# Optimization experiments

Hardware: AMD Instinct MI355X
Metric: run time of the kernel (lower is better)

## Reference

```python
import jax, jax.numpy as jnp
import numpy as np
import math

N = 6000      # nodes
E = 96000     # edges
HID = 32      # hidden_dim
DEPTH = 3
RATIO = 0.2
BN_EPS = 1e-5


def _gcn(x, A, W, b):
    # GCNConv(improved=True): A_hat = A + 2I, out = D^-1/2 A_hat D^-1/2 (x W) + b
    # A[i, j] = weight of edge j -> i (message-passing orientation)
    n = A.shape[0]
    idx = jnp.arange(n)
    Ah = A.at[idx, idx].add(2.0)
    deg = Ah.sum(axis=1)
    dinv = jnp.where(deg > 0, jax.lax.rsqrt(deg), 0.0)
    An = dinv[:, None] * Ah * dinv[None, :]
    return An @ (x @ W) + b


def _two_hop(A):
    # GraphUNet.augment_adj: add self loops, sparse A@A, remove self loops
    n = A.shape[0]
    idx = jnp.arange(n)
    A1 = A.at[idx, idx].add(1.0)
    A2 = A1 @ A1
    return A2.at[idx, idx].set(0.0)


def _unpack(fl):
    x = fl[0]
    wd = list(fl[1:9:2]); bd = list(fl[2:9:2])
    pv = list(fl[9:12])
    wu = list(fl[12:18:2]); bu = list(fl[13:18:2])
    return x, (wd, bd, pv, wu, bu, fl[18], fl[19])


def _forward(x, edge_index, params):
    wd, bd, pv, wu, bu, bn_g, bn_b = params
    n = x.shape[0]
    # dense adjacency, transposed so A[dst, src] = edge weight
    A = jnp.zeros((n, n), x.dtype).at[edge_index[1], edge_index[0]].add(1.0)
    h = jax.nn.relu(_gcn(x, A, wd[0], bd[0]))
    xs, As, perms = [h], [A], []
    Acur = A
    for i in range(DEPTH):
        A2 = _two_hop(Acur)
        # TopKPooling: score = tanh(x.p / ||p||), keep top ceil(ratio*n)
        p = pv[i]
        score = jnp.tanh((h @ p) / jnp.linalg.norm(p))
        k = math.ceil(RATIO * h.shape[0])
        vals, perm = jax.lax.top_k(score, k)
        h = h[perm] * vals[:, None]
        Acur = A2[perm][:, perm]
        h = jax.nn.relu(_gcn(h, Acur, wd[i + 1], bd[i + 1]))
        if i < DEPTH - 1:
            xs.append(h)
            As.append(Acur)
        perms.append(perm)
    for i in range(DEPTH):
        j = DEPTH - 1 - i
        up = jnp.zeros_like(xs[j]).at[perms[j]].set(h)  # unpool
        h = _gcn(xs[j] + up, As[j], wu[i], bu[i])       # sum_res=True
        if i < DEPTH - 1:
            h = jax.nn.relu(h)
    # PFNet5 tail: BatchNorm1d(1) (batch stats) + sigmoid on channel 0
    v = h[:, 0]
    mean = v.mean()
    var = jnp.mean((v - mean) ** 2)
    r1 = jax.nn.sigmoid(bn_g[0] * (v - mean) * jax.lax.rsqrt(var + BN_EPS) + bn_b[0])
    return h.at[:, 0].set(r1)


def setup_inputs() -> dict:
    key = jax.random.key(0)
    ks = jax.random.split(key, 20)
    def nrm(k, shape, s=0.1):
        return jax.random.normal(k, shape, jnp.float32) * s
    inp = {
        "x": jax.random.normal(ks[0], (N, 3), jnp.float32),
        "edge_index": jax.random.randint(ks[1], (2, E), 0, N),
    }
    dims_down = [(3, HID), (HID, HID), (HID, HID), (HID, HID)]
    for i, (di, do) in enumerate(dims_down):
        inp[f"w_down{i}"] = nrm(ks[2 + i], (di, do))
        inp[f"b_down{i}"] = jnp.zeros((do,), jnp.float32)
    for i in range(3):
        inp[f"pool{i}"] = nrm(ks[6 + i], (HID,))
    dims_up = [(HID, HID), (HID, HID), (HID, 4)]
    for i, (di, do) in enumerate(dims_up):
        inp[f"w_up{i}"] = nrm(ks[9 + i], (di, do))
        inp[f"b_up{i}"] = jnp.zeros((do,), jnp.float32)
    inp["bn_gamma"] = jnp.ones((1,), jnp.float32)
    inp["bn_beta"] = jnp.zeros((1,), jnp.float32)
    return inp


def reference(x, edge_index, w_down0, b_down0, w_down1, b_down1, w_down2, b_down2,
              w_down3, b_down3, pool0, pool1, pool2, w_up0, b_up0, w_up1, b_up1,
              w_up2, b_up2, bn_gamma, bn_beta):
    fl = (x, w_down0, b_down0, w_down1, b_down1, w_down2, b_down2, w_down3, b_down3,
          pool0, pool1, pool2, w_up0, b_up0, w_up1, b_up1, w_up2, b_up2,
          bn_gamma, bn_beta)
    x_, params = _unpack(fl)
    return _forward(x_, edge_index, params)
```

## Files before the change

### kernel.cpp

```cpp
#include <hip/hip_runtime.h>
#include <hip/hip_bf16.h>

#define TPB 256

__global__ void k_count(const int* __restrict__ ei, int E, int* __restrict__ cnt){
  int e = blockIdx.x*blockDim.x + threadIdx.x;
  if(e < E) atomicAdd(&cnt[ei[E + e]], 1);
}

template<int IPT>
__global__ void k_scan(const int* __restrict__ cnt, int n, int* __restrict__ rowptr){
  int tid = threadIdx.x;
  int base = tid * IPT;
  int loc[IPT]; int s = 0;
  #pragma unroll
  for(int q = 0; q < IPT; ++q){ int i = base + q; int v = (i < n) ? cnt[i] : 0; s += v; loc[q] = s; }
  int lane = tid & 63, w = tid >> 6;
  int ss = s;
  #pragma unroll
  for(int o = 1; o < 64; o <<= 1){ int t = __shfl_up(ss, o, 64); if(lane >= o) ss += t; }
  __shared__ int wsum[16];
  if(lane == 63) wsum[w] = ss;
  __syncthreads();
  if(tid < 16){
    int t = wsum[tid];
    for(int o = 1; o < 16; o <<= 1){ int u = __shfl_up(t, o, 64); if(tid >= o) t += u; }
    wsum[tid] = t;
  }
  __syncthreads();
  int excl = ss - s + (w > 0 ? wsum[w-1] : 0);
  if(tid == 0) rowptr[0] = 0;
  #pragma unroll
  for(int q = 0; q < IPT; ++q){ int i = base + q; if(i < n) rowptr[i+1] = excl + loc[q]; }
}

__global__ void k_fill(const int* __restrict__ ei, int E, const int* __restrict__ rowptr,
                       int* __restrict__ fill, int* __restrict__ colidx){
  int e = blockIdx.x*blockDim.x + threadIdx.x;
  if(e >= E) return;
  int d = ei[E + e], s = ei[e];
  int p = rowptr[d] + atomicAdd(&fill[d], 1);
  colidx[p] = s;
}

__global__ void k_mm_dinv(const float* __restrict__ h, const float* __restrict__ W,
                          const float* __restrict__ dinv, const int* __restrict__ cnt,
                          float* __restrict__ dinv_out, float* __restrict__ out,
                          int n, int cin, int cout){
  int t = blockIdx.x*blockDim.x + threadIdx.x;
  if(t >= n*cout) return;
  int i = t / cout, c = t - i*cout;
  float dv;
  if(cnt){ dv = rsqrtf((float)cnt[i] + 2.0f); if(c == 0) dinv_out[i] = dv; }
  else dv = dinv[i];
  float s = 0.f;
  for(int d = 0; d < cin; ++d) s += h[i*cin + d] * W[d*cout + c];
  out[t] = dv * s;
}

template<int COUT>
__global__ void k_addup_mm(const float* __restrict__ base, const float* __restrict__ h,
                           const int* __restrict__ rank, const float* __restrict__ W,
                           const float* __restrict__ dinv, float* __restrict__ out, int n){
  int t = blockIdx.x*blockDim.x + threadIdx.x;
  if(t >= n*COUT) return;
  int i = t / COUT, c = t - i*COUT;
  int r = rank[i];
  const float* br = base + (size_t)i*32;
  const float* hr = h + (size_t)(r >= 0 ? r : 0)*32;
  float s = 0.f;
  #pragma unroll
  for(int d = 0; d < 32; ++d){
    float z = br[d] + ((r >= 0) ? hr[d] : 0.f);
    s += z * W[d*COUT + c];
  }
  out[t] = dinv[i] * s;
}

template<int C, bool RELU, bool SCORE>
__global__ void k_csr_gcn(const int* __restrict__ rowptr, const int* __restrict__ colidx,
                          const float* __restrict__ xwd, const float* __restrict__ dinv,
                          const float* __restrict__ bias, float* __restrict__ out, int n,
                          const float* __restrict__ pvec, float* __restrict__ score){
  int t = blockIdx.x*blockDim.x + threadIdx.x;
  if(t >= n*C) return;
  int i = t / C, c = t % C;
  float acc = 2.0f * xwd[i*C + c];
  int b = rowptr[i], e = rowptr[i+1];
  for(int p = b; p < e; ++p) acc += xwd[colidx[p]*C + c];
  float y = dinv[i]*acc + bias[c];
  y = RELU ? fmaxf(y, 0.f) : y;
  out[t] = y;
  if(SCORE){
    float pv = pvec[c];
    float sd = y*pv, nn = pv*pv;
    #pragma unroll
    for(int o = 16; o > 0; o >>= 1){ sd += __shfl_xor(sd, o, 32); nn += __shfl_xor(nn, o, 32); }
    if(c == 0) score[i] = tanhf(sd / sqrtf(nn));
  }
}

template<int NMAX>
__global__ __launch_bounds__(1024)
void k_pool_radix(const float* __restrict__ score, const float* __restrict__ h,
                  int n, int k, int* __restrict__ perm, int* __restrict__ rank,
                  float* __restrict__ hout){
  __shared__ unsigned keys[NMAX];
  __shared__ int bins[2048];
  __shared__ int wsum[16];
  __shared__ unsigned s_prefix;
  __shared__ int s_rk, s_found, s_cntgt;
  int tid = threadIdx.x, lane = tid & 63, w = tid >> 6;

  for(int i = tid; i < n; i += 1024){
    rank[i] = -1;
    unsigned u = __float_as_uint(score[i]);
    u ^= (u & 0x80000000u) ? 0xFFFFFFFFu : 0x80000000u;
    keys[i] = u;
  }
  if(tid == 0){ s_prefix = 0u; s_rk = k; }
  __syncthreads();

  for(int pass = 0; pass < 3; ++pass){
    const int width = (pass < 2) ? 11 : 10;
    const int shift = (pass == 0) ? 21 : ((pass == 1) ? 10 : 0);
    const int nb = 1 << width;
    for(int b2 = tid; b2 < nb; b2 += 1024) bins[b2] = 0;
    __syncthreads();
    unsigned prefix = s_prefix;
    int rk = s_rk;
    const int hs = shift + width;
    for(int i = tid; i < n; i += 1024){
      unsigned kk = keys[i];
      bool match = (pass == 0) || ((kk >> hs) == (prefix >> hs));
      if(match) atomicAdd(&bins[(kk >> shift) & (nb-1)], 1);
    }
    __syncthreads();
    int ipt = (nb + 1023) >> 10;
    int loc0 = 0, loc1 = 0, s = 0;
    { int r = tid*ipt; int v = (r < nb) ? bins[nb-1-r] : 0; s += v; loc0 = s;
      if(ipt == 2){ int r2 = r+1; int v2 = (r2 < nb) ? bins[nb-1-r2] : 0; s += v2; loc1 = s; } }
    int ss = s;
    #pragma unroll
    for(int o = 1; o < 64; o <<= 1){ int t2 = __shfl_up(ss, o, 64); if(lane >= o) ss += t2; }
    if(lane == 63) wsum[w] = ss;
    __syncthreads();
    if(tid < 16){
      int t2 = wsum[tid];
      #pragma unroll
      for(int o = 1; o < 16; o <<= 1){ int u2 = __shfl_up(t2, o, 64); if(tid >= o) t2 += u2; }
      wsum[tid] = t2;
    }
    __syncthreads();
    int excl = ss - s + (w ? wsum[w-1] : 0);
    { int r = tid*ipt; if(r < nb) bins[nb-1-r] = excl + loc0;
      if(ipt == 2){ int r2 = r+1; if(r2 < nb) bins[nb-1-r2] = excl + loc1; } }
    __syncthreads();
    for(int b2 = tid; b2 < nb; b2 += 1024){
      int cge = bins[b2];
      int cgt = (b2+1 < nb) ? bins[b2+1] : 0;
      if(cge >= rk && cgt < rk){ s_found = b2; s_cntgt = cgt; }
    }
    __syncthreads();
    if(tid == 0){ s_prefix |= ((unsigned)s_found) << shift; s_rk -= s_cntgt; }
    __syncthreads();
  }
  unsigned T = s_prefix;
  int r = s_rk;
  int cgt_total = k - r;

  int CH = (n + 1023) >> 10;
  int base = tid*CH, c_gt = 0, c_eq = 0;
  for(int q = 0; q < CH; ++q){
    int i = base+q;
    if(i < n){ unsigned u = keys[i]; c_gt += (u > T); c_eq += (u == T); }
  }
  int packed = c_gt*8192 + c_eq;
  int ss2 = packed;
  #pragma unroll
  for(int o = 1; o < 64; o <<= 1){ int t2 = __shfl_up(ss2, o, 64); if(lane >= o) ss2 += t2; }
  if(lane == 63) wsum[w] = ss2;
  __syncthreads();
  if(tid < 16){
    int t2 = wsum[tid];
    #pragma unroll
    for(int o = 1; o < 16; o <<= 1){ int u2 = __shfl_up(t2, o, 64); if(tid >= o) t2 += u2; }
    wsum[tid] = t2;
  }
  __syncthreads();
  int excl2 = ss2 - packed + (w ? wsum[w-1] : 0);
  int gt_before = excl2 / 8192, eq_before = excl2 % 8192;
  for(int q = 0; q < CH; ++q){
    int i = base+q;
    if(i >= n) continue;
    unsigned u = keys[i];
    if(u > T){ int pos = gt_before++; perm[pos] = i; rank[i] = pos; }
    else if(u == T){
      int tr = eq_before++;
      if(tr < r){ int pos = cgt_total + tr; perm[pos] = i; rank[i] = pos; }
    }
  }
  __syncthreads();
  for(int t = tid; t < k*32; t += 1024){
    int i = t >> 5, c = t & 31;
    int idx = perm[i];
    hout[t] = h[(size_t)idx*32 + c] * score[idx];
  }
}

__global__ __launch_bounds__(256)
void k_build_B1(const int* __restrict__ rowptr, const int* __restrict__ colidx,
                const int* __restrict__ perm1, const int* __restrict__ rank1, int K1,
                float* __restrict__ dinv1, int* __restrict__ rowbeg, int* __restrict__ rowend,
                int* __restrict__ col1, float* __restrict__ val1, int* __restrict__ cursor){
  __shared__ float row[1216];
  __shared__ int wsum[4];
  __shared__ float fs[4];
  __shared__ int s_base;
  int tid = threadIdx.x, lane = tid & 63, w = tid >> 6;
  int i = blockIdx.x;
  for(int j = tid; j < K1; j += 256) row[j] = 0.f;
  __syncthreads();
  int d = perm1[i];
  int b = rowptr[d], len = rowptr[d+1]-b;
  for(int p = tid; p < len; p += 256){
    int s = colidx[b+p]; int rs = rank1[s];
    if(rs >= 0) atomicAdd(&row[rs], 2.0f);
  }
  for(int ww = tid; ww < len*8; ww += 256){
    int p = ww >> 3, sub = ww & 7;
    int s = colidx[b+p];
    for(int q = rowptr[s]+sub, qe = rowptr[s+1]; q < qe; q += 8){
      int r2 = rank1[colidx[q]];
      if(r2 >= 0) atomicAdd(&row[r2], 1.0f);
    }
  }
  __syncthreads();
  if(tid == 0) row[i] = 0.f;
  __syncthreads();
  float s = 0.f;
  for(int j = tid; j < K1; j += 256) s += row[j];
  for(int o = 32; o > 0; o >>= 1) s += __shfl_down(s, o, 64);
  if(lane == 0) fs[w] = s;
  __syncthreads();
  if(tid == 0){
    dinv1[i] = rsqrtf(fs[0]+fs[1]+fs[2]+fs[3] + 2.0f);
    row[i] = 1.0f;
  }
  __syncthreads();
  int CH = (K1 + 255) >> 8;
  int base = tid*CH, cnt = 0;
  for(int q = 0; q < CH; ++q){ int j = base+q; if(j < K1 && row[j] != 0.f) ++cnt; }
  int ss = cnt;
  #pragma unroll
  for(int o = 1; o < 64; o <<= 1){ int t2 = __shfl_up(ss, o, 64); if(lane >= o) ss += t2; }
  if(lane == 63) wsum[w] = ss;
  __syncthreads();
  if(tid < 4){
    int t2 = wsum[tid];
    for(int o = 1; o < 4; o <<= 1){ int u2 = __shfl_up(t2, o, 64); if(tid >= o) t2 += u2; }
    wsum[tid] = t2;
  }
  __syncthreads();
  if(tid == 0) s_base = atomicAdd(cursor, wsum[3]);
  __syncthreads();
  int off = s_base + ss - cnt + (w ? wsum[w-1] : 0);
  for(int q = 0; q < CH; ++q){
    int j = base+q;
    if(j < K1 && row[j] != 0.f){ col1[off] = j; val1[off] = row[j]; ++off; }
  }
  if(tid == 0){ rowbeg[i] = s_base; rowend[i] = s_base + wsum[3]; }
}

template<bool RELU, bool SCORE>
__global__ void k_spmm_gcn(const int* __restrict__ rb, const int* __restrict__ re,
                           const int* __restrict__ ci, const float* __restrict__ cv,
                           const float* __restrict__ hwd, const float* __restrict__ dinv,
                           const float* __restrict__ bias, float* __restrict__ out, int n,
                           const float* __restrict__ pvec, float* __restrict__ score){
  int t = blockIdx.x*blockDim.x + threadIdx.x;
  if(t >= n*32) return;
  int i = t >> 5, c = t & 31;
  float acc = hwd[i*32 + c];
  for(int p = rb[i], e = re[i]; p < e; ++p) acc += cv[p]*hwd[ci[p]*32 + c];
  float y = dinv[i]*acc + bias[c];
  y = RELU ? fmaxf(y, 0.f) : y;
  out[t] = y;
  if(SCORE){
    float pv = pvec[c];
    float sd = y*pv, nn = pv*pv;
    #pragma unroll
    for(int o = 16; o > 0; o >>= 1){ sd += __shfl_xor(sd, o, 32); nn += __shfl_xor(nn, o, 32); }
    if(c == 0) score[i] = tanhf(sd / sqrtf(nn));
  }
}

__global__ __launch_bounds__(256)
void k_twohop_sp(const int* __restrict__ rb, const int* __restrict__ re,
                 const int* __restrict__ ci, const float* __restrict__ cv,
                 const int* __restrict__ perm2, const int* __restrict__ rank2,
                 float* __restrict__ C2, float* __restrict__ dinv2, int K2){
  __shared__ float acc[256];
  __shared__ float fs[4];
  int i = blockIdx.x, tid = threadIdx.x, lane = tid & 63, w = tid >> 6;
  for(int j = tid; j < K2; j += 256) acc[j] = 0.f;
  __syncthreads();
  int qi = perm2[i];
  int b = rb[qi], len = re[qi]-b;
  for(int ww = tid; ww < len*8; ww += 256){
    int p = b + (ww >> 3), sub = ww & 7;
    int t = ci[p]; float v = cv[p];
    for(int q = rb[t] + sub, qe = re[t]; q < qe; q += 8){
      int j = rank2[ci[q]];
      if(j >= 0) atomicAdd(&acc[j], v*cv[q]);
    }
  }
  __syncthreads();
  if(tid == 0) acc[i] = 0.f;
  __syncthreads();
  float s = 0.f;
  for(int j = tid; j < K2; j += 256) s += acc[j];
  for(int o = 32; o > 0; o >>= 1) s += __shfl_down(s, o, 64);
  if(lane == 0) fs[w] = s;
  __syncthreads();
  if(tid == 0) dinv2[i] = rsqrtf(fs[0]+fs[1]+fs[2]+fs[3] + 2.0f);
  for(int j = tid; j < K2; j += 256) C2[(size_t)i*K2 + j] = acc[j];
}

template<bool RELU, bool SCORE>
__global__ void k_dgcn_row(const float* __restrict__ C, const float* __restrict__ hwd,
                           const float* __restrict__ dinv, const float* __restrict__ bias,
                           float* __restrict__ out, int n,
                           const float* __restrict__ pvec, float* __restrict__ score){
  __shared__ float sh[8][32];
  int i = blockIdx.x;
  int c = threadIdx.x & 31, s = threadIdx.x >> 5;
  const float* row = C + (size_t)i*n;
  float acc = 0.f;
  for(int t = s; t < n; t += 8) acc += row[t]*hwd[t*32 + c];
  sh[s][c] = acc;
  __syncthreads();
  if(s == 0){
    float a = sh[0][c]+sh[1][c]+sh[2][c]+sh[3][c]+sh[4][c]+sh[5][c]+sh[6][c]+sh[7][c];
    a += 2.f*hwd[i*32 + c];
    float y = dinv[i]*a + bias[c];
    y = RELU ? fmaxf(y, 0.f) : y;
    out[i*32 + c] = y;
    if(SCORE){
      float pv = pvec[c];
      float sd = y*pv, nn = pv*pv;
      #pragma unroll
      for(int o = 16; o > 0; o >>= 1){ sd += __shfl_xor(sd, o, 32); nn += __shfl_xor(nn, o, 32); }
      if(c == 0) score[i] = tanhf(sd / sqrtf(nn));
    }
  }
}

__global__ __launch_bounds__(256)
void k_twohop_d3(const float* __restrict__ C2, int n, const int* __restrict__ perm3,
                 int k, float* __restrict__ C3, float* __restrict__ dinv3){
  __shared__ float acc[4][64];
  int i = blockIdx.x, tid = threadIdx.x;
  int col = tid & 63, st = tid >> 6;
  int qi = perm3[i];
  int qj = (col < k) ? perm3[col] : 0;
  float a = 0.f;
  if(col < k){
    for(int tt = st; tt < n; tt += 4){
      float av = C2[(size_t)qi*n + tt] + ((tt == qi) ? 1.f : 0.f);
      float bv = C2[(size_t)tt*n + qj] + ((tt == qj) ? 1.f : 0.f);
      a += av * bv;
    }
  }
  acc[st][col] = a;
  __syncthreads();
  if(st == 0){
    float v = acc[0][col]+acc[1][col]+acc[2][col]+acc[3][col];
    if(col == i) v = 0.f;
    if(col < k) C3[(size_t)i*k + col] = v;
    float sv = (col < k) ? v : 0.f;
    for(int o = 32; o > 0; o >>= 1) sv += __shfl_down(sv, o, 64);
    if(col == 0) dinv3[i] = rsqrtf(sv + 2.0f);
  }
}

__global__ void k_bn(float* __restrict__ out, int n, const float* __restrict__ g,
                     const float* __restrict__ b){
  __shared__ float sh[16];
  __shared__ float sval;
  int tid = threadIdx.x, lane = tid & 63, w = tid >> 6;
  int nw = blockDim.x >> 6;
  float s = 0.f;
  for(int i = tid; i < n; i += blockDim.x) s += out[i*4];
  for(int o = 32; o > 0; o >>= 1) s += __shfl_down(s, o, 64);
  if(lane == 0) sh[w] = s;
  __syncthreads();
  if(tid == 0){ float t = 0.f; for(int q = 0; q < nw; ++q) t += sh[q]; sval = t / n; }
  __syncthreads();
  float mean = sval;
  float v = 0.f;
  for(int i = tid; i < n; i += blockDim.x){ float d = out[i*4] - mean; v += d*d; }
  for(int o = 32; o > 0; o >>= 1) v += __shfl_down(v, o, 64);
  __syncthreads();
  if(lane == 0) sh[w] = v;
  __syncthreads();
  if(tid == 0){ float t = 0.f; for(int q = 0; q < nw; ++q) t += sh[q]; sval = t / n; }
  __syncthreads();
  float var = sval;
  float scale = g[0] * rsqrtf(var + 1e-5f);
  float beta = b[0];
  for(int i = tid; i < n; i += blockDim.x){
    float r = scale*(out[i*4] - mean) + beta;
    out[i*4] = 1.f / (1.f + expf(-r));
  }
}

extern "C" void kernel_launch(void* const* d_in, const int* in_sizes, int n_in,
                              void* d_out, int out_size, void* d_ws, size_t ws_size,
                              hipStream_t stream){
  const float* x  =(const float*)d_in[0];
  const int*   ei =(const int*)  d_in[1];
  const float* W0 =(const float*)d_in[2];  const float* b0 =(const float*)d_in[3];
  const float* W1 =(const float*)d_in[4];  const float* b1 =(const float*)d_in[5];
  const float* W2 =(const float*)d_in[6];  const float* b2 =(const float*)d_in[7];
  const float* W3 =(const float*)d_in[8];  const float* b3 =(const float*)d_in[9];
  const float* p0 =(const float*)d_in[10];
  const float* p1 =(const float*)d_in[11];
  const float* p2 =(const float*)d_in[12];
  const float* Wu0=(const float*)d_in[13]; const float* bu0=(const float*)d_in[14];
  const float* Wu1=(const float*)d_in[15]; const float* bu1=(const float*)d_in[16];
  const float* Wu2=(const float*)d_in[17]; const float* bu2=(const float*)d_in[18];
  const float* bng=(const float*)d_in[19]; const float* bnb=(const float*)d_in[20];
  float* out = (float*)d_out;

  const int n0 = in_sizes[0] / 3;
  const int E  = in_sizes[1] / 2;
  const int K1 = (n0 + 4) / 5;
  const int K2 = (K1 + 4) / 5;
  const int K3 = (K2 + 4) / 5;
  const int CAP1 = 512*1024;

  char* wsp = (char*)d_ws; size_t off = 0;
  auto alloc = [&](size_t bytes)->char*{
    char* p = wsp + off; off = (off + bytes + 255) & ~((size_t)255); return p;
  };

  int*   zreg   = (int*)  alloc((size_t)(2*n0+64)*4);
  int*   cnt    = zreg;
  int*   fill   = zreg + n0;
  int*   cursor = zreg + 2*n0;
  int*   rowptr = (int*)  alloc((size_t)(n0+1)*4);
  int*   colidx = (int*)  alloc((size_t)E*4);
  float* dinv0  = (float*)alloc((size_t)n0*4);
  float* hwd    = (float*)alloc((size_t)n0*32*4);
  float* h0     = (float*)alloc((size_t)n0*32*4);
  float* score  = (float*)alloc((size_t)n0*4);
  int*   perm1  = (int*)  alloc((size_t)K1*4);
  int*   rank1  = (int*)  alloc((size_t)n0*4);
  float* h1p    = (float*)alloc((size_t)K1*32*4);
  float* dinv1  = (float*)alloc((size_t)K1*4);
  int*   rowbeg1= (int*)  alloc((size_t)K1*4);
  int*   rowend1= (int*)  alloc((size_t)K1*4);
  int*   col1   = (int*)  alloc((size_t)CAP1*4);
  float* val1   = (float*)alloc((size_t)CAP1*4);
  float* h1     = (float*)alloc((size_t)K1*32*4);
  int*   perm2  = (int*)  alloc((size_t)K2*4);
  int*   rank2  = (int*)  alloc((size_t)K1*4);
  float* h2p    = (float*)alloc((size_t)K2*32*4);
  float* C2     = (float*)alloc((size_t)K2*K2*4);
  float* dinv2  = (float*)alloc((size_t)K2*4);
  float* h2     = (float*)alloc((size_t)K2*32*4);
  int*   perm3  = (int*)  alloc((size_t)K3*4);
  int*   rank3  = (int*)  alloc((size_t)K2*4);
  float* h3p    = (float*)alloc((size_t)K3*32*4);
  float* C3     = (float*)alloc((size_t)K3*K3*4);
  float* dinv3  = (float*)alloc((size_t)K3*4);
  float* h3     = (float*)alloc((size_t)K3*32*4);
  float* hu2    = (float*)alloc((size_t)K2*32*4);
  float* hu1    = (float*)alloc((size_t)K1*32*4);

  hipMemsetAsync(zreg, 0, (size_t)(2*n0+64)*4, stream);

  const int gE = (E + TPB - 1) / TPB;
  k_count  <<<gE, TPB, 0, stream>>>(ei, E, cnt);
  k_scan<6><<<1, 1024, 0, stream>>>(cnt, n0, rowptr);
  k_fill   <<<gE, TPB, 0, stream>>>(ei, E, rowptr, fill, colidx);
  k_mm_dinv<<<(n0*32+TPB-1)/TPB, TPB, 0, stream>>>(x, W0, nullptr, cnt, dinv0, hwd, n0, 3, 32);
  k_csr_gcn<32,true,true><<<(n0*32+TPB-1)/TPB, TPB, 0, stream>>>(rowptr, colidx, hwd, dinv0, b0, h0, n0, p0, score);
  k_pool_radix<6144><<<1, 1024, 0, stream>>>(score, h0, n0, K1, perm1, rank1, h1p);
  k_build_B1<<<K1, 256, 0, stream>>>(rowptr, colidx, perm1, rank1, K1,
                                     dinv1, rowbeg1, rowend1, col1, val1, cursor);
  k_mm_dinv<<<(K1*32+TPB-1)/TPB, TPB, 0, stream>>>(h1p, W1, dinv1, nullptr, nullptr, hwd, K1, 32, 32);
  k_spmm_gcn<true,true><<<(K1*32+TPB-1)/TPB, TPB, 0, stream>>>(rowbeg1, rowend1, col1, val1, hwd, dinv1, b1, h1, K1, p1, score);
  k_pool_radix<1216><<<1, 1024, 0, stream>>>(score, h1, K1, K2, perm2, rank2, h2p);
  k_twohop_sp<<<K2, 256, 0, stream>>>(rowbeg1, rowend1, col1, val1, perm2, rank2, C2, dinv2, K2);
  k_mm_dinv<<<(K2*32+TPB-1)/TPB, TPB, 0, stream>>>(h2p, W2, dinv2, nullptr, nullptr, hwd, K2, 32, 32);
  k_dgcn_row<true,true><<<K2, 256, 0, stream>>>(C2, hwd, dinv2, b2, h2, K2, p2, score);
  k_pool_radix<256><<<1, 1024, 0, stream>>>(score, h2, K2, K3, perm3, rank3, h3p);
  k_twohop_d3<<<K3, 256, 0, stream>>>(C2, K2, perm3, K3, C3, dinv3);
  k_mm_dinv<<<(K3*32+TPB-1)/TPB, TPB, 0, stream>>>(h3p, W3, dinv3, nullptr, nullptr, hwd, K3, 32, 32);
  k_dgcn_row<true,false><<<K3, 256, 0, stream>>>(C3, hwd, dinv3, b3, h3, K3, nullptr, nullptr);
  k_addup_mm<32><<<(K2*32+TPB-1)/TPB, TPB, 0, stream>>>(h2, h3, rank3, Wu0, dinv2, hwd, K2);
  k_dgcn_row<true,false><<<K2, 256, 0, stream>>>(C2, hwd, dinv2, bu0, hu2, K2, nullptr, nullptr);
  k_addup_mm<32><<<(K1*32+TPB-1)/TPB, TPB, 0, stream>>>(h1, hu2, rank2, Wu1, dinv1, hwd, K1);
  k_spmm_gcn<true,false><<<(K1*32+TPB-1)/TPB, TPB, 0, stream>>>(rowbeg1, rowend1, col1, val1, hwd, dinv1, bu1, hu1, K1, nullptr, nullptr);
  k_addup_mm<4><<<(n0*4+TPB-1)/TPB, TPB, 0, stream>>>(h0, hu1, rank1, Wu2, dinv0, hwd, n0);
  k_csr_gcn<4,false,false><<<(n0*4+TPB-1)/TPB, TPB, 0, stream>>>(rowptr, colidx, hwd, dinv0, bu2, out, n0, nullptr, nullptr);
  k_bn<<<1, 1024, 0, stream>>>(out, n0, bng, bnb);
}
```

Baseline: 246.1 us.

## Fuse weight matmuls into pooling and aggregation, parallelize batchnorm reduction

```diff
diff --git a/kernel.cpp b/kernel.cpp
--- a/kernel.cpp
+++ b/kernel.cpp
@@ -2,6 +2,16 @@
 #include <hip/hip_bf16.h>
 
 #define TPB 256
+
+__device__ __forceinline__ float block_sum_f(float v, float* fs){
+  int tid = threadIdx.x, lane = tid & 63, w = tid >> 6;
+  #pragma unroll
+  for(int o = 32; o > 0; o >>= 1) v += __shfl_down(v, o, 64);
+  __syncthreads();
+  if(lane == 0) fs[w] = v;
+  __syncthreads();
+  return fs[0] + fs[1] + fs[2] + fs[3];
+}
 
 __global__ void k_count(const int* __restrict__ ei, int E, int* __restrict__ cnt){
   int e = blockIdx.x*blockDim.x + threadIdx.x;
@@ -24,7 +34,7 @@
   __syncthreads();
   if(tid < 16){
     int t = wsum[tid];
-    for(int o = 1; o < 16; o <<= 1){ int u = __shfl_up(t, o, 64); if(tid >= o) t += u; }
+    for(int o = 1; o < 16; o <<= 1){ int uu = __shfl_up(t, o, 64); if(tid >= o) t += uu; }
     wsum[tid] = t;
   }
   __syncthreads();
@@ -43,84 +53,57 @@
   colidx[p] = s;
 }
 
-__global__ void k_mm_dinv(const float* __restrict__ h, const float* __restrict__ W,
-                          const float* __restrict__ dinv, const int* __restrict__ cnt,
-                          float* __restrict__ dinv_out, float* __restrict__ out,
-                          int n, int cin, int cout){
+__global__ void k_agg3(const float* __restrict__ x, const int* __restrict__ cnt,
+                       const int* __restrict__ rowptr, const int* __restrict__ colidx,
+                       float* __restrict__ dinv0, float* __restrict__ xa, int n){
+  int i = blockIdx.x*blockDim.x + threadIdx.x;
+  if(i >= n) return;
+  float di = rsqrtf((float)cnt[i] + 2.0f);
+  dinv0[i] = di;
+  float s0 = 2.f*di*x[i*3], s1 = 2.f*di*x[i*3+1], s2 = 2.f*di*x[i*3+2];
+  for(int q = rowptr[i]; q < rowptr[i+1]; ++q){
+    int j = colidx[q];
+    float dj = rsqrtf((float)cnt[j] + 2.0f);
+    s0 += dj*x[j*3]; s1 += dj*x[j*3+1]; s2 += dj*x[j*3+2];
+  }
+  xa[i*3] = s0; xa[i*3+1] = s1; xa[i*3+2] = s2;
+}
+
+__global__ void k_gcn0(const float* __restrict__ xa, const float* __restrict__ W0,
+                       const float* __restrict__ b0, const float* __restrict__ dinv0,
+                       const float* __restrict__ p0, float* __restrict__ h0,
+                       float* __restrict__ score, int n){
   int t = blockIdx.x*blockDim.x + threadIdx.x;
-  if(t >= n*cout) return;
-  int i = t / cout, c = t - i*cout;
-  float dv;
-  if(cnt){ dv = rsqrtf((float)cnt[i] + 2.0f); if(c == 0) dinv_out[i] = dv; }
-  else dv = dinv[i];
-  float s = 0.f;
-  for(int d = 0; d < cin; ++d) s += h[i*cin + d] * W[d*cout + c];
-  out[t] = dv * s;
-}
-
-template<int COUT>
-__global__ void k_addup_mm(const float* __restrict__ base, const float* __restrict__ h,
-                           const int* __restrict__ rank, const float* __restrict__ W,
-                           const float* __restrict__ dinv, float* __restrict__ out, int n){
-  int t = blockIdx.x*blockDim.x + threadIdx.x;
-  if(t >= n*COUT) return;
-  int i = t / COUT, c = t - i*COUT;
-  int r = rank[i];
-  const float* br = base + (size_t)i*32;
-  const float* hr = h + (size_t)(r >= 0 ? r : 0)*32;
-  float s = 0.f;
-  #pragma unroll
-  for(int d = 0; d < 32; ++d){
-    float z = br[d] + ((r >= 0) ? hr[d] : 0.f);
-    s += z * W[d*COUT + c];
-  }
-  out[t] = dinv[i] * s;
-}
-
-template<int C, bool RELU, bool SCORE>
-__global__ void k_csr_gcn(const int* __restrict__ rowptr, const int* __restrict__ colidx,
-                          const float* __restrict__ xwd, const float* __restrict__ dinv,
-                          const float* __restrict__ bias, float* __restrict__ out, int n,
-                          const float* __restrict__ pvec, float* __restrict__ score){
-  int t = blockIdx.x*blockDim.x + threadIdx.x;
-  if(t >= n*C) return;
-  int i = t / C, c = t % C;
-  float acc = 2.0f * xwd[i*C + c];
-  int b = rowptr[i], e = rowptr[i+1];
-  for(int p = b; p < e; ++p) acc += xwd[colidx[p]*C + c];
-  float y = dinv[i]*acc + bias[c];
-  y = RELU ? fmaxf(y, 0.f) : y;
-  out[t] = y;
-  if(SCORE){
-    float pv = pvec[c];
-    float sd = y*pv, nn = pv*pv;
-    #pragma unroll
-    for(int o = 16; o > 0; o >>= 1){ sd += __shfl_xor(sd, o, 32); nn += __shfl_xor(nn, o, 32); }
-    if(c == 0) score[i] = tanhf(sd / sqrtf(nn));
-  }
+  if(t >= n*32) return;
+  int i = t >> 5, c = t & 31;
+  float y = dinv0[i]*(xa[i*3]*W0[c] + xa[i*3+1]*W0[32+c] + xa[i*3+2]*W0[64+c]) + b0[c];
+  y = fmaxf(y, 0.f);
+  h0[t] = y;
+  float pv = p0[c]; float sd = y*pv, nn = pv*pv;
+  #pragma unroll
+  for(int o = 16; o > 0; o >>= 1){ sd += __shfl_xor(sd, o, 32); nn += __shfl_xor(nn, o, 32); }
+  if(c == 0) score[i] = tanhf(sd / sqrtf(nn));
 }
 
 template<int NMAX>
 __global__ __launch_bounds__(1024)
-void k_pool_radix(const float* __restrict__ score, const float* __restrict__ h,
-                  int n, int k, int* __restrict__ perm, int* __restrict__ rank,
-                  float* __restrict__ hout){
+void k_pool(const float* __restrict__ score, const float* __restrict__ h,
+            const float* __restrict__ W, int n, int k,
+            int* __restrict__ perm, int* __restrict__ rank, float* __restrict__ hw){
   __shared__ unsigned keys[NMAX];
   __shared__ int bins[2048];
   __shared__ int wsum[16];
   __shared__ unsigned s_prefix;
   __shared__ int s_rk, s_found, s_cntgt;
   int tid = threadIdx.x, lane = tid & 63, w = tid >> 6;
-
   for(int i = tid; i < n; i += 1024){
     rank[i] = -1;
-    unsigned u = __float_as_uint(score[i]);
-    u ^= (u & 0x80000000u) ? 0xFFFFFFFFu : 0x80000000u;
-    keys[i] = u;
+    unsigned uu = __float_as_uint(score[i]);
+    uu ^= (uu & 0x80000000u) ? 0xFFFFFFFFu : 0x80000000u;
+    keys[i] = uu;
   }
   if(tid == 0){ s_prefix = 0u; s_rk = k; }
   __syncthreads();
-
   for(int pass = 0; pass < 3; ++pass){
     const int width = (pass < 2) ? 11 : 10;
     const int shift = (pass == 0) ? 21 : ((pass == 1) ? 10 : 0);
@@ -168,12 +151,11 @@
   unsigned T = s_prefix;
   int r = s_rk;
   int cgt_total = k - r;
-
   int CH = (n + 1023) >> 10;
   int base = tid*CH, c_gt = 0, c_eq = 0;
   for(int q = 0; q < CH; ++q){
     int i = base+q;
-    if(i < n){ unsigned u = keys[i]; c_gt += (u > T); c_eq += (u == T); }
+    if(i < n){ unsigned uu = keys[i]; c_gt += (uu > T); c_eq += (uu == T); }
   }
   int packed = c_gt*8192 + c_eq;
   int ss2 = packed;
@@ -193,9 +175,9 @@
   for(int q = 0; q < CH; ++q){
     int i = base+q;
     if(i >= n) continue;
-    unsigned u = keys[i];
-    if(u > T){ int pos = gt_before++; perm[pos] = i; rank[i] = pos; }
-    else if(u == T){
+    unsigned uu = keys[i];
+    if(uu > T){ int pos = gt_before++; perm[pos] = i; rank[i] = pos; }
+    else if(uu == T){
       int tr = eq_before++;
       if(tr < r){ int pos = cgt_total + tr; perm[pos] = i; rank[i] = pos; }
     }
@@ -204,7 +186,12 @@
   for(int t = tid; t < k*32; t += 1024){
     int i = t >> 5, c = t & 31;
     int idx = perm[i];
-    hout[t] = h[(size_t)idx*32 + c] * score[idx];
+    float sc = score[idx];
+    const float* hr = h + (size_t)idx*32;
+    float s = 0.f;
+    #pragma unroll
+    for(int d = 0; d < 32; ++d) s += hr[d]*W[d*32 + c];
+    hw[t] = sc*s;
   }
 }
 
@@ -240,13 +227,8 @@
   __syncthreads();
   float s = 0.f;
   for(int j = tid; j < K1; j += 256) s += row[j];
-  for(int o = 32; o > 0; o >>= 1) s += __shfl_down(s, o, 64);
-  if(lane == 0) fs[w] = s;
-  __syncthreads();
-  if(tid == 0){
-    dinv1[i] = rsqrtf(fs[0]+fs[1]+fs[2]+fs[3] + 2.0f);
-    row[i] = 1.0f;
-  }
+  float tot = block_sum_f(s, fs);
+  if(tid == 0){ dinv1[i] = rsqrtf(tot + 2.0f); row[i] = 1.0f; }
   __syncthreads();
   int CH = (K1 + 255) >> 8;
   int base = tid*CH, cnt = 0;
@@ -273,16 +255,20 @@
 }
 
 template<bool RELU, bool SCORE>
-__global__ void k_spmm_gcn(const int* __restrict__ rb, const int* __restrict__ re,
-                           const int* __restrict__ ci, const float* __restrict__ cv,
-                           const float* __restrict__ hwd, const float* __restrict__ dinv,
-                           const float* __restrict__ bias, float* __restrict__ out, int n,
-                           const float* __restrict__ pvec, float* __restrict__ score){
+__global__ void k_spmm(const int* __restrict__ rb, const int* __restrict__ re,
+                       const int* __restrict__ ci, const float* __restrict__ cv,
+                       const float* __restrict__ hw, const float* __restrict__ dinv,
+                       const float* __restrict__ bias, float* __restrict__ out, int n,
+                       const float* __restrict__ pvec, float* __restrict__ score,
+                       int* __restrict__ rankinit){
   int t = blockIdx.x*blockDim.x + threadIdx.x;
   if(t >= n*32) return;
   int i = t >> 5, c = t & 31;
-  float acc = hwd[i*32 + c];
-  for(int p = rb[i], e = re[i]; p < e; ++p) acc += cv[p]*hwd[ci[p]*32 + c];
+  float acc = dinv[i]*hw[t];
+  for(int p = rb[i], e = re[i]; p < e; ++p){
+    int j = ci[p];
+    acc += cv[p]*dinv[j]*hw[j*32 + c];
+  }
   float y = dinv[i]*acc + bias[c];
   y = RELU ? fmaxf(y, 0.f) : y;
   out[t] = y;
@@ -293,6 +279,7 @@
     for(int o = 16; o > 0; o >>= 1){ sd += __shfl_xor(sd, o, 32); nn += __shfl_xor(nn, o, 32); }
     if(c == 0) score[i] = tanhf(sd / sqrtf(nn));
   }
+  if(rankinit && c == 0) rankinit[i] = -1;
 }
 
 __global__ __launch_bounds__(256)
@@ -302,7 +289,7 @@
                  float* __restrict__ C2, float* __restrict__ dinv2, int K2){
   __shared__ float acc[256];
   __shared__ float fs[4];
-  int i = blockIdx.x, tid = threadIdx.x, lane = tid & 63, w = tid >> 6;
+  int i = blockIdx.x, tid = threadIdx.x;
   for(int j = tid; j < K2; j += 256) acc[j] = 0.f;
   __syncthreads();
   int qi = perm2[i];
@@ -320,30 +307,29 @@
   __syncthreads();
   float s = 0.f;
   for(int j = tid; j < K2; j += 256) s += acc[j];
-  for(int o = 32; o > 0; o >>= 1) s += __shfl_down(s, o, 64);
-  if(lane == 0) fs[w] = s;
-  __syncthreads();
-  if(tid == 0) dinv2[i] = rsqrtf(fs[0]+fs[1]+fs[2]+fs[3] + 2.0f);
+  float tot = block_sum_f(s, fs);
+  if(tid == 0) dinv2[i] = rsqrtf(tot + 2.0f);
   for(int j = tid; j < K2; j += 256) C2[(size_t)i*K2 + j] = acc[j];
 }
 
 template<bool RELU, bool SCORE>
-__global__ void k_dgcn_row(const float* __restrict__ C, const float* __restrict__ hwd,
-                           const float* __restrict__ dinv, const float* __restrict__ bias,
-                           float* __restrict__ out, int n,
-                           const float* __restrict__ pvec, float* __restrict__ score){
+__global__ __launch_bounds__(256)
+void k_dgcn(const float* __restrict__ C, const float* __restrict__ hw,
+            const float* __restrict__ dinv, const float* __restrict__ bias,
+            float* __restrict__ out, int n, const float* __restrict__ pvec,
+            float* __restrict__ score, int* __restrict__ rankinit){
   __shared__ float sh[8][32];
   int i = blockIdx.x;
-  int c = threadIdx.x & 31, s = threadIdx.x >> 5;
+  int c = threadIdx.x & 31, sg = threadIdx.x >> 5;
   const float* row = C + (size_t)i*n;
-  float acc = 0.f;
-  for(int t = s; t < n; t += 8) acc += row[t]*hwd[t*32 + c];
-  sh[s][c] = acc;
-  __syncthreads();
-  if(s == 0){
-    float a = sh[0][c]+sh[1][c]+sh[2][c]+sh[3][c]+sh[4][c]+sh[5][c]+sh[6][c]+sh[7][c];
-    a += 2.f*hwd[i*32 + c];
-    float y = dinv[i]*a + bias[c];
+  float a = 0.f;
+  for(int t = sg; t < n; t += 8) a += row[t]*dinv[t]*hw[t*32 + c];
+  sh[sg][c] = a;
+  __syncthreads();
+  if(sg == 0){
+    float aa = sh[0][c]+sh[1][c]+sh[2][c]+sh[3][c]+sh[4][c]+sh[5][c]+sh[6][c]+sh[7][c];
+    aa += 2.f*dinv[i]*hw[i*32 + c];
+    float y = dinv[i]*aa + bias[c];
     y = RELU ? fmaxf(y, 0.f) : y;
     out[i*32 + c] = y;
     if(SCORE){
@@ -353,6 +339,7 @@
       for(int o = 16; o > 0; o >>= 1){ sd += __shfl_xor(sd, o, 32); nn += __shfl_xor(nn, o, 32); }
       if(c == 0) score[i] = tanhf(sd / sqrtf(nn));
     }
+    if(rankinit && c == 0) rankinit[i] = -1;
   }
 }
 
@@ -379,39 +366,67 @@
     if(col == i) v = 0.f;
     if(col < k) C3[(size_t)i*k + col] = v;
     float sv = (col < k) ? v : 0.f;
+    #pragma unroll
     for(int o = 32; o > 0; o >>= 1) sv += __shfl_down(sv, o, 64);
     if(col == 0) dinv3[i] = rsqrtf(sv + 2.0f);
   }
 }
 
-__global__ void k_bn(float* __restrict__ out, int n, const float* __restrict__ g,
-                     const float* __restrict__ b){
-  __shared__ float sh[16];
-  __shared__ float sval;
-  int tid = threadIdx.x, lane = tid & 63, w = tid >> 6;
-  int nw = blockDim.x >> 6;
+template<int COUT, bool DINV>
+__global__ void k_addup_mm(const float* __restrict__ base, const float* __restrict__ h,
+                           const int* __restrict__ rank, const float* __restrict__ W,
+                           const float* __restrict__ dinv, float* __restrict__ out, int n){
+  int t = blockIdx.x*blockDim.x + threadIdx.x;
+  if(t >= n*COUT) return;
+  int i = t / COUT, c = t - i*COUT;
+  int r = rank[i];
+  const float* br = base + (size_t)i*32;
+  const float* hr = h + (size_t)(r >= 0 ? r : 0)*32;
   float s = 0.f;
-  for(int i = tid; i < n; i += blockDim.x) s += out[i*4];
-  for(int o = 32; o > 0; o >>= 1) s += __shfl_down(s, o, 64);
-  if(lane == 0) sh[w] = s;
-  __syncthreads();
-  if(tid == 0){ float t = 0.f; for(int q = 0; q < nw; ++q) t += sh[q]; sval = t / n; }
-  __syncthreads();
-  float mean = sval;
-  float v = 0.f;
-  for(int i = tid; i < n; i += blockDim.x){ float d = out[i*4] - mean; v += d*d; }
-  for(int o = 32; o > 0; o >>= 1) v += __shfl_down(v, o, 64);
-  __syncthreads();
-  if(lane == 0) sh[w] = v;
-  __syncthreads();
-  if(tid == 0){ float t = 0.f; for(int q = 0; q < nw; ++q) t += sh[q]; sval = t / n; }
-  __syncthreads();
-  float var = sval;
-  float scale = g[0] * rsqrtf(var + 1e-5f);
-  float beta = b[0];
-  for(int i = tid; i < n; i += blockDim.x){
+  #pragma unroll
+  for(int d = 0; d < 32; ++d){
+    float z = br[d] + ((r >= 0) ? hr[d] : 0.f);
+    s += z * W[d*COUT + c];
+  }
+  out[t] = DINV ? (dinv[i]*s) : s;
+}
+
+__global__ void k_gcn_final(const int* __restrict__ rowptr, const int* __restrict__ colidx,
+                            const float* __restrict__ hw4, const float* __restrict__ dinv0,
+                            const float* __restrict__ bias, float* __restrict__ out, int n,
+                            float* __restrict__ bnp, float* __restrict__ bnq){
+  __shared__ float fs[4];
+  int t = blockIdx.x*blockDim.x + threadIdx.x;
+  float vs = 0.f, vq = 0.f;
+  if(t < n*4){
+    int i = t >> 2, c = t & 3;
+    float acc = 2.f*hw4[t];
+    for(int q = rowptr[i]; q < rowptr[i+1]; ++q) acc += hw4[colidx[q]*4 + c];
+    float y = dinv0[i]*acc + bias[c];
+    out[t] = y;
+    if(c == 0){ vs = y; vq = y*y; }
+  }
+  float bs = block_sum_f(vs, fs);
+  float bq = block_sum_f(vq, fs);
+  if(threadIdx.x == 0){ bnp[blockIdx.x] = bs; bnq[blockIdx.x] = bq; }
+}
+
+__global__ void k_bn_finish(float* __restrict__ out, int n, int nblk,
+                            const float* __restrict__ bnp, const float* __restrict__ bnq,
+                            const float* __restrict__ g, const float* __restrict__ b){
+  __shared__ float fs[4];
+  int tid = threadIdx.x;
+  float sv = (tid < nblk) ? bnp[tid] : 0.f;
+  float qv = (tid < nblk) ? bnq[tid] : 0.f;
+  float tsum = block_sum_f(sv, fs);
+  float tsq  = block_sum_f(qv, fs);
+  float mean = tsum / n;
+  float var  = tsq / n - mean*mean;
+  float scale = g[0]*rsqrtf(var + 1e-5f);
+  float beta  = b[0];
+  for(int i = blockIdx.x*blockDim.x + tid; i < n; i += gridDim.x*blockDim.x){
     float r = scale*(out[i*4] - mean) + beta;
-    out[i*4] = 1.f / (1.f + expf(-r));
+    out[i*4] = 1.f/(1.f + expf(-r));
   }
 }
 
@@ -447,17 +462,17 @@
 
   int*   zreg   = (int*)  alloc((size_t)(2*n0+64)*4);
   int*   cnt    = zreg;
-  int*   fill   = zreg + n0;
+  int*   fillc  = zreg + n0;
   int*   cursor = zreg + 2*n0;
   int*   rowptr = (int*)  alloc((size_t)(n0+1)*4);
   int*   colidx = (int*)  alloc((size_t)E*4);
   float* dinv0  = (float*)alloc((size_t)n0*4);
-  float* hwd    = (float*)alloc((size_t)n0*32*4);
+  float* xa     = (float*)alloc((size_t)n0*3*4);
   float* h0     = (float*)alloc((size_t)n0*32*4);
   float* score  = (float*)alloc((size_t)n0*4);
   int*   perm1  = (int*)  alloc((size_t)K1*4);
   int*   rank1  = (int*)  alloc((size_t)n0*4);
-  float* h1p    = (float*)alloc((size_t)K1*32*4);
+  float* hw1    = (float*)alloc((size_t)K1*32*4);
   float* dinv1  = (float*)alloc((size_t)K1*4);
   int*   rowbeg1= (int*)  alloc((size_t)K1*4);
   int*   rowend1= (int*)  alloc((size_t)K1*4);
@@ -466,45 +481,48 @@
   float* h1     = (float*)alloc((size_t)K1*32*4);
   int*   perm2  = (int*)  alloc((size_t)K2*4);
   int*   rank2  = (int*)  alloc((size_t)K1*4);
-  float* h2p    = (float*)alloc((size_t)K2*32*4);
+  float* hw2    = (float*)alloc((size_t)K2*32*4);
   float* C2     = (float*)alloc((size_t)K2*K2*4);
   float* dinv2  = (float*)alloc((size_t)K2*4);
   float* h2     = (float*)alloc((size_t)K2*32*4);
   int*   perm3  = (int*)  alloc((size_t)K3*4);
   int*   rank3  = (int*)  alloc((size_t)K2*4);
-  float* h3p    = (float*)alloc((size_t)K3*32*4);
+  float* hw3    = (float*)alloc((size_t)K3*32*4);
   float* C3     = (float*)alloc((size_t)K3*K3*4);
   float* dinv3  = (float*)alloc((size_t)K3*4);
   float* h3     = (float*)alloc((size_t)K3*32*4);
   float* hu2    = (float*)alloc((size_t)K2*32*4);
   float* hu1    = (float*)alloc((size_t)K1*32*4);
+  float* hw4    = (float*)alloc((size_t)n0*4*4);
+  float* bnp    = (float*)alloc((size_t)128*4);
+  float* bnq    = (float*)alloc((size_t)128*4);
 
   hipMemsetAsync(zreg, 0, (size_t)(2*n0+64)*4, stream);
 
-  const int gE = (E + TPB - 1) / TPB;
+  const int gE  = (E + TPB - 1) / TPB;
+  const int gBN = (n0*4 + TPB - 1) / TPB;
   k_count  <<<gE, TPB, 0, stream>>>(ei, E, cnt);
   k_scan<6><<<1, 1024, 0, stream>>>(cnt, n0, rowptr);
-  k_fill   <<<gE, TPB, 0, stream>>>(ei, E, rowptr, fill, colidx);
-  k_mm_dinv<<<(n0*32+TPB-1)/TPB, TPB, 0, stream>>>(x, W0, nullptr, cnt, dinv0, hwd, n0, 3, 32);
-  k_csr_gcn<32,true,true><<<(n0*32+TPB-1)/TPB, TPB, 0, stream>>>(rowptr, colidx, hwd, dinv0, b0, h0, n0, p0, score);
-  k_pool_radix<6144><<<1, 1024, 0, stream>>>(score, h0, n0, K1, perm1, rank1, h1p);
+  k_fill   <<<gE, TPB, 0, stream>>>(ei, E, rowptr, fillc, colidx);
+  k_agg3<<<(n0+TPB-1)/TPB, TPB, 0, stream>>>(x, cnt, rowptr, colidx, dinv0, xa, n0);
+  k_gcn0<<<(n0*32+TPB-1)/TPB, TPB, 0, stream>>>(xa, W0, b0, dinv0, p0, h0, score, n0);
+  k_pool<6144><<<1, 1024, 0, stream>>>(score, h0, W1, n0, K1, perm1, rank1, hw1);
   k_build_B1<<<K1, 256, 0, stream>>>(rowptr, colidx, perm1, rank1, K1,
                                      dinv1, rowbeg1, rowend1, col1, val1, cursor);
-  k_mm_dinv<<<(K1*32+TPB-1)/TPB, TPB, 0, stream>>>(h1p, W1, dinv1, nullptr, nullptr, hwd, K1, 32, 32);
-  k_spmm_gcn<true,true><<<(K1*32+TPB-1)/TPB, TPB, 0, stream>>>(rowbeg1, rowend1, col1, val1, hwd, dinv1, b1, h1, K1, p1, score);
-  k_pool_radix<1216><<<1, 1024, 0, stream>>>(score, h1, K1, K2, perm2, rank2, h2p);
+  k_spmm<true,true><<<(K1*32+TPB-1)/TPB, TPB, 0, stream>>>(rowbeg1, rowend1, col1, val1,
+                                                           hw1, dinv1, b1, h1, K1, p1, score, rank2);
+  k_pool<1216><<<1, 1024, 0, stream>>>(score, h1, W2, K1, K2, perm2, rank2, hw2);
   k_twohop_sp<<<K2, 256, 0, stream>>>(rowbeg1, rowend1, col1, val1, perm2, rank2, C2, dinv2, K2);
-  k_mm_dinv<<<(K2*32+TPB-1)/TPB, TPB, 0, stream>>>(h2p, W2, dinv2, nullptr, nullptr, hwd, K2, 32, 32);
-  k_dgcn_row<true,true><<<K2, 256, 0, stream>>>(C2, hwd, dinv2, b2, h2, K2, p2, score);
-  k_pool_radix<256><<<1, 1024, 0, stream>>>(score, h2, K2, K3, perm3, rank3, h3p);
+  k_dgcn<true,true><<<K2, 256, 0, stream>>>(C2, hw2, dinv2, b2, h2, K2, p2, score, rank3);
+  k_pool<256><<<1, 1024, 0, stream>>>(score, h2, W3, K2, K3, perm3, rank3, hw3);
   k_twohop_d3<<<K3, 256, 0, stream>>>(C2, K2, perm3, K3, C3, dinv3);
-  k_mm_dinv<<<(K3*32+TPB-1)/TPB, TPB, 0, stream>>>(h3p, W3, dinv3, nullptr, nullptr, hwd, K3, 32, 32);
-  k_dgcn_row<true,false><<<K3, 256, 0, stream>>>(C3, hwd, dinv3, b3, h3, K3, nullptr, nullptr);
-  k_addup_mm<32><<<(K2*32+TPB-1)/TPB, TPB, 0, stream>>>(h2, h3, rank3, Wu0, dinv2, hwd, K2);
-  k_dgcn_row<true,false><<<K2, 256, 0, stream>>>(C2, hwd, dinv2, bu0, hu2, K2, nullptr, nullptr);
-  k_addup_mm<32><<<(K1*32+TPB-1)/TPB, TPB, 0, stream>>>(h1, hu2, rank2, Wu1, dinv1, hwd, K1);
-  k_spmm_gcn<true,false><<<(K1*32+TPB-1)/TPB, TPB, 0, stream>>>(rowbeg1, rowend1, col1, val1, hwd, dinv1, bu1, hu1, K1, nullptr, nullptr);
-  k_addup_mm<4><<<(n0*4+TPB-1)/TPB, TPB, 0, stream>>>(h0, hu1, rank1, Wu2, dinv0, hwd, n0);
-  k_csr_gcn<4,false,false><<<(n0*4+TPB-1)/TPB, TPB, 0, stream>>>(rowptr, colidx, hwd, dinv0, bu2, out, n0, nullptr, nullptr);
-  k_bn<<<1, 1024, 0, stream>>>(out, n0, bng, bnb);
-}
+  k_dgcn<true,false><<<K3, 256, 0, stream>>>(C3, hw3, dinv3, b3, h3, K3, nullptr, nullptr, nullptr);
+  k_addup_mm<32,false><<<(K2*32+TPB-1)/TPB, TPB, 0, stream>>>(h2, h3, rank3, Wu0, nullptr, hw2, K2);
+  k_dgcn<true,false><<<K2, 256, 0, stream>>>(C2, hw2, dinv2, bu0, hu2, K2, nullptr, nullptr, nullptr);
+  k_addup_mm<32,false><<<(K1*32+TPB-1)/TPB, TPB, 0, stream>>>(h1, hu2, rank2, Wu1, nullptr, hw1, K1);
+  k_spmm<true,false><<<(K1*32+TPB-1)/TPB, TPB, 0, stream>>>(rowbeg1, rowend1, col1, val1,
+                                                            hw1, dinv1, bu1, hu1, K1, nullptr, nullptr, nullptr);
+  k_addup_mm<4,true><<<(n0*4+TPB-1)/TPB, TPB, 0, stream>>>(h0, hu1, rank1, Wu2, dinv0, hw4, n0);
+  k_gcn_final<<<gBN, TPB, 0, stream>>>(rowptr, colidx, hw4, dinv0, bu2, out, n0, bnp, bnq);
+  k_bn_finish<<<24, TPB, 0, stream>>>(out, n0, gBN, bnp, bnq, bng, bnb);
+}
```

Measured after the change: 260.4 us. 5.8% more time.
